# Optimization experiments

Measured on AMD Instinct MI355X. Metric: run time of the kernel, lower is better.

Reference implementation:

```python
import jax, jax.numpy as jnp
import numpy as np

B, S, D, H = 4, 2048, 1024, 16
HD = D // H  # head size = 64


def setup_inputs() -> dict:
    key = jax.random.key(0)
    ks = jax.random.split(key, 8)
    scale = 1.0 / np.sqrt(D)
    return {
        "q": jax.random.normal(ks[0], (B, S, D), jnp.float32),
        "k": jax.random.normal(ks[1], (B, S, D), jnp.float32),
        "v": jax.random.normal(ks[2], (B, S, D), jnp.float32),
        "mask": jnp.ones((B, 1, S), dtype=bool),
        "Wq": jax.random.normal(ks[3], (D, D), jnp.float32) * scale,
        "bq": jnp.zeros((D,), jnp.float32),
        "Wk": jax.random.normal(ks[4], (D, D), jnp.float32) * scale,
        "bk": jnp.zeros((D,), jnp.float32),
        "Wv": jax.random.normal(ks[5], (D, D), jnp.float32) * scale,
        "bv": jnp.zeros((D,), jnp.float32),
        "Wo": jax.random.normal(ks[6], (D, D), jnp.float32) * scale,
        "bo": jnp.zeros((D,), jnp.float32),
    }


def _split_heads(x):
    # [B, S, D] -> [B, H, S, HD]
    return x.reshape(B, -1, H, HD).transpose(0, 2, 1, 3)


def reference(q, k, v, mask, Wq, bq, Wk, bk, Wv, bv, Wo, bo):
    qh = _split_heads(q @ Wq + bq) / jnp.sqrt(jnp.asarray(HD, q.dtype))
    kh = _split_heads(k @ Wk + bk)
    vh = _split_heads(v @ Wv + bv)
    # scores: [B, H, Sq, Sk]
    scores = jnp.einsum("bhqd,bhkd->bhqk", qh, kh)
    neg_inf = jnp.asarray(-jnp.inf, scores.dtype)
    scores = jnp.where(mask[:, None, :, :], scores, neg_inf)
    attn = jax.nn.softmax(scores, axis=-1)
    # dropout p=0.0 -> identity (eval semantics)
    ctx = jnp.einsum("bhqk,bhkd->bhqd", attn, vh)
    ctx = ctx.transpose(0, 2, 1, 3).reshape(B, -1, D)
    return ctx @ Wo + bo
```

## Files before the change

kernel.cpp:

```cpp
#include <hip/hip_runtime.h>
#include <hip/hip_bf16.h>


typedef __bf16 bf16_t;
typedef __bf16 bf16x8 __attribute__((ext_vector_type(8)));
typedef __bf16 bf16x4 __attribute__((ext_vector_type(4)));
typedef float  floatx4 __attribute__((ext_vector_type(4)));

constexpr int B_ = 4, S_ = 2048, D_ = 1024, H_ = 16, HD_ = 64;
constexpr int M_ = B_ * S_;

#if defined(__has_builtin)
#if __has_builtin(__builtin_amdgcn_exp2f)
#define EXP2_RAW __builtin_amdgcn_exp2f
#endif
#endif
#ifndef EXP2_RAW
#define EXP2_RAW __builtin_exp2f
#endif

__device__ __forceinline__ void gll16(const void* gsrc, void* ldst) {
  __builtin_amdgcn_global_load_lds(
      (__attribute__((address_space(1))) void*)gsrc,
      (__attribute__((address_space(3))) void*)ldst, 16, 0, 0);
}

struct WPtrs { const float* src[4]; bf16_t* dst[4]; };

__global__ __launch_bounds__(256)
void transpose_cast_w(WPtrs p) {
  __shared__ float tile[64][65];
  const int m  = blockIdx.y;
  const int kt = blockIdx.x >> 4;
  const int nt = blockIdx.x & 15;
  const float* W  = p.src[m];
  bf16_t*      Wt = p.dst[m];
  const int t = threadIdx.x;
#pragma unroll
  for (int i = 0; i < 16; ++i) {
    int idx = i*256 + t;
    int r = idx >> 6, c = idx & 63;
    tile[r][c] = W[(kt*64 + r)*D_ + nt*64 + c];
  }
  __syncthreads();
#pragma unroll
  for (int i = 0; i < 16; ++i) {
    int idx = i*256 + t;
    int r = idx >> 6, c = idx & 63;
    Wt[(long)(nt*64 + r)*D_ + kt*64 + c] = (bf16_t)tile[c][r];
  }
}

struct ProjArgs {
  const float*  A[3];
  const bf16_t* Bt[3];
  const float*  bias[3];
  float         scale[3];
  void*         out[3];
  int           epi[3];
};

__global__ __launch_bounds__(256)
void proj_gemm(ProjArgs pa) {
  __shared__ alignas(16) bf16_t AsT[128*72];
  __shared__ alignas(16) char   Bs[128*64*2];

  const int z    = blockIdx.z;
  const int tid  = threadIdx.x;
  const int lane = tid & 63;
  const int w    = tid >> 6;
  const int quad = lane >> 4;
  const int l16  = lane & 15;
  const int wr   = w >> 1, wc = w & 1;
  const long row0 = (long)blockIdx.x * 128;
  const int  col0 = blockIdx.y * 128;

  const float*  A  = pa.A[z];
  const bf16_t* Bt = pa.Bt[z];

  floatx4 acc[4][4];
#pragma unroll
  for (int i = 0; i < 4; ++i)
#pragma unroll
    for (int j = 0; j < 4; ++j) { floatx4 zz = {0.f,0.f,0.f,0.f}; acc[i][j] = zz; }

  for (int kt = 0; kt < D_/64; ++kt) {
    const int k0 = kt * 64;
#pragma unroll
    for (int i = 0; i < 8; ++i) {
      int g = i*256 + tid;
      int r = g >> 4, c4 = g & 15;
      float4 f = *(const float4*)(A + (row0 + r)*D_ + k0 + c4*4);
      bf16x4 pk;
      pk[0]=(bf16_t)f.x; pk[1]=(bf16_t)f.y; pk[2]=(bf16_t)f.z; pk[3]=(bf16_t)f.w;
      *(bf16x4*)(AsT + r*72 + c4*4) = pk;
    }
#pragma unroll
    for (int it = 0; it < 4; ++it) {
      int chunk = it*4 + w;
      int g = chunk*64 + lane;
      int r = g >> 3, cs = g & 7;
      int cg = cs ^ (r & 7);
      gll16(Bt + (long)(col0 + r)*D_ + k0 + cg*8, Bs + chunk*1024);
    }
    __syncthreads();

#pragma unroll
    for (int ks = 0; ks < 2; ++ks) {
      bf16x8 a[4], b[4];
#pragma unroll
      for (int i = 0; i < 4; ++i) {
        int r = wr*64 + i*16 + l16;
        a[i] = *(const bf16x8*)(AsT + r*72 + (ks*4 + quad)*8);
      }
#pragma unroll
      for (int j = 0; j < 4; ++j) {
        int r = wc*64 + j*16 + l16;
        int c = ks*4 + quad;
        b[j] = *(const bf16x8*)(Bs + ((r*8) + (c ^ (r & 7)))*16);
      }
#pragma unroll
      for (int i = 0; i < 4; ++i)
#pragma unroll
        for (int j = 0; j < 4; ++j)
          acc[i][j] = __builtin_amdgcn_mfma_f32_16x16x32_bf16(a[i], b[j], acc[i][j], 0, 0, 0);
    }
    __syncthreads();
  }

  const float* bias = pa.bias[z];
  const float scale = pa.scale[z];
  if (pa.epi[z] == 0) {
    bf16_t* C = (bf16_t*)pa.out[z];
#pragma unroll
    for (int j = 0; j < 4; ++j) {
      int c = col0 + wc*64 + j*16 + l16;
      float bv = bias[c];
#pragma unroll
      for (int i = 0; i < 4; ++i) {
        long r = row0 + wr*64 + i*16 + quad*4;
#pragma unroll
        for (int rg = 0; rg < 4; ++rg)
          C[(r+rg)*D_ + c] = (bf16_t)((acc[i][j][rg] + bv) * scale);
      }
    }
  } else {
    bf16_t* VT = (bf16_t*)pa.out[z];
#pragma unroll
    for (int j = 0; j < 4; ++j) {
      int c  = col0 + wc*64 + j*16 + l16;
      int h  = c >> 6, hd = c & 63;
      float bv = bias[c];
#pragma unroll
      for (int i = 0; i < 4; ++i) {
        long r = row0 + wr*64 + i*16 + quad*4;
        int b = (int)(r >> 11), s = (int)(r & 2047);
        bf16x4 pk;
#pragma unroll
        for (int rg = 0; rg < 4; ++rg) pk[rg] = (bf16_t)(acc[i][j][rg] + bv);
        *(bf16x4*)(VT + ((long)((b*H_ + h)*HD_ + hd))*S_ + s) = pk;
      }
    }
  }
}

__global__ __launch_bounds__(256)
void out_gemm(const bf16_t* __restrict__ Ap, const bf16_t* __restrict__ Bt,
              const float* __restrict__ bias, float* __restrict__ Cp)
{
  __shared__ alignas(16) char smem[128*64*2 + 128*64*2];
  char* As = smem;
  char* Bs = smem + 128*64*2;

  const int tid  = threadIdx.x;
  const int lane = tid & 63;
  const int w    = tid >> 6;
  const int quad = lane >> 4;
  const int l16  = lane & 15;
  const int wr   = w >> 1, wc = w & 1;
  const long row0 = (long)blockIdx.x * 128;
  const int  col0 = blockIdx.y * 128;

  floatx4 acc[4][4];
#pragma unroll
  for (int i = 0; i < 4; ++i)
#pragma unroll
    for (int j = 0; j < 4; ++j) { floatx4 zz = {0.f,0.f,0.f,0.f}; acc[i][j] = zz; }

  for (int kt = 0; kt < D_/64; ++kt) {
    const int k0 = kt * 64;
#pragma unroll
    for (int it = 0; it < 4; ++it) {
      int chunk = it*4 + w;
      int g = chunk*64 + lane;
      int r = g >> 3, cs = g & 7;
      int cg = cs ^ (r & 7);
      gll16(Ap + (long)(row0 + r)*D_ + k0 + cg*8, As + chunk*1024);
    }
#pragma unroll
    for (int it = 0; it < 4; ++it) {
      int chunk = it*4 + w;
      int g = chunk*64 + lane;
      int r = g >> 3, cs = g & 7;
      int cg = cs ^ (r & 7);
      gll16(Bt + (long)(col0 + r)*D_ + k0 + cg*8, Bs + chunk*1024);
    }
    __syncthreads();

#pragma unroll
    for (int ks = 0; ks < 2; ++ks) {
      bf16x8 a[4], b[4];
#pragma unroll
      for (int i = 0; i < 4; ++i) {
        int r = wr*64 + i*16 + l16;
        int c = ks*4 + quad;
        a[i] = *(const bf16x8*)(As + ((r*8) + (c ^ (r & 7)))*16);
      }
#pragma unroll
      for (int j = 0; j < 4; ++j) {
        int r = wc*64 + j*16 + l16;
        int c = ks*4 + quad;
        b[j] = *(const bf16x8*)(Bs + ((r*8) + (c ^ (r & 7)))*16);
      }
#pragma unroll
      for (int i = 0; i < 4; ++i)
#pragma unroll
        for (int j = 0; j < 4; ++j)
          acc[i][j] = __builtin_amdgcn_mfma_f32_16x16x32_bf16(a[i], b[j], acc[i][j], 0, 0, 0);
    }
    __syncthreads();
  }

#pragma unroll
  for (int j = 0; j < 4; ++j) {
    int c = col0 + wc*64 + j*16 + l16;
    float bv = bias[c];
#pragma unroll
    for (int i = 0; i < 4; ++i) {
      long r = row0 + wr*64 + i*16 + quad*4;
#pragma unroll
      for (int rg = 0; rg < 4; ++rg)
        Cp[(r+rg)*D_ + c] = acc[i][j][rg] + bv;
    }
  }
}

__global__ __launch_bounds__(256, 2)
void attn(const bf16_t* __restrict__ Qp, const bf16_t* __restrict__ Kp,
          const bf16_t* __restrict__ VTg, bf16_t* __restrict__ Ctx)
{
  __shared__ alignas(16) bf16_t Ks [2][128*64];
  __shared__ alignas(16) bf16_t VTs[2][64*128];
  __shared__ alignas(16) bf16_t Ps [4][32*64];

  const int tid  = threadIdx.x;
  const int lane = tid & 63;
  const int w    = tid >> 6;
  const int quad = lane >> 4;
  const int l16  = lane & 15;

  const int h  = blockIdx.x;
  const int qt = blockIdx.y;
  const int b  = blockIdx.z;
  const int bh = b*H_ + h;
  const long rowQ0 = (long)b * S_ + qt*128;
  const int  colH  = h * HD_;

  bf16x8 qf[2][2];
#pragma unroll
  for (int ks = 0; ks < 2; ++ks)
#pragma unroll
    for (int qs = 0; qs < 2; ++qs)
      qf[ks][qs] = *(const bf16x8*)(Qp + (rowQ0 + w*32 + qs*16 + l16)*D_ + colH + ks*32 + quad*8);

  floatx4 O[4][2];
#pragma unroll
  for (int vb = 0; vb < 4; ++vb)
#pragma unroll
    for (int qs = 0; qs < 2; ++qs) { floatx4 zz = {0.f,0.f,0.f,0.f}; O[vb][qs] = zz; }
  float lsum[2] = {0.f, 0.f};

  bf16_t* Pw = &Ps[w][0];

  {
    const long rowK0 = (long)b * S_;
#pragma unroll
    for (int i = 0; i < 4; ++i) {
      int chunk = w*4 + i;
      int G = chunk*64 + lane;
      int r = G >> 3, cs = G & 7, cg = cs ^ (r & 7);
      gll16(Kp + (rowK0 + r)*D_ + colH + cg*8, (char*)Ks[0] + chunk*1024);
    }
#pragma unroll
    for (int i = 0; i < 4; ++i) {
      int chunk = w*4 + i;
      int G = chunk*64 + lane;
      int r = G >> 4, cs = G & 15, cg = cs ^ (r & 15);
      gll16(VTg + ((long)(bh*HD_ + r))*S_ + cg*8, (char*)VTs[0] + chunk*1024);
    }
  }

  for (int kt = 0; kt < S_/128; ++kt) {
    __syncthreads();
    const int bs = kt & 1;

    if (kt + 1 < S_/128) {
      const int  kn    = kt + 1, bn = kn & 1;
      const int  kv0n  = kn*128;
      const long rowK0 = (long)b * S_ + kv0n;
#pragma unroll
      for (int i = 0; i < 4; ++i) {
        int chunk = w*4 + i;
        int G = chunk*64 + lane;
        int r = G >> 3, cs = G & 7, cg = cs ^ (r & 7);
        gll16(Kp + (rowK0 + r)*D_ + colH + cg*8, (char*)Ks[bn] + chunk*1024);
      }
#pragma unroll
      for (int i = 0; i < 4; ++i) {
        int chunk = w*4 + i;
        int G = chunk*64 + lane;
        int r = G >> 4, cs = G & 15, cg = cs ^ (r & 15);
        gll16(VTg + ((long)(bh*HD_ + r))*S_ + kv0n + cg*8, (char*)VTs[bn] + chunk*1024);
      }
    }

    floatx4 sc[8][2];
#pragma unroll
    for (int nb = 0; nb < 8; ++nb)
#pragma unroll
      for (int qs = 0; qs < 2; ++qs) { floatx4 zz = {0.f,0.f,0.f,0.f}; sc[nb][qs] = zz; }
#pragma unroll
    for (int ks = 0; ks < 2; ++ks) {
#pragma unroll
      for (int nb = 0; nb < 8; ++nb) {
        bf16x8 a = *(const bf16x8*)(Ks[bs] + (nb*16 + l16)*64 + (((ks*4 + quad) ^ (l16 & 7))*8));
#pragma unroll
        for (int qs = 0; qs < 2; ++qs)
          sc[nb][qs] = __builtin_amdgcn_mfma_f32_16x16x32_bf16(a, qf[ks][qs], sc[nb][qs], 0, 0, 0);
      }
    }

#pragma unroll
    for (int half = 0; half < 2; ++half) {
#pragma unroll
      for (int nbl = 0; nbl < 4; ++nbl) {
        int nb = half*4 + nbl;
#pragma unroll
        for (int qs = 0; qs < 2; ++qs) {
          bf16x4 pk;
#pragma unroll
          for (int rg = 0; rg < 4; ++rg) {
            float p = EXP2_RAW(sc[nb][qs][rg]);
            lsum[qs] += p;
            pk[rg] = (bf16_t)p;
          }
          *(bf16x4*)(Pw + (qs*16 + l16)*64 + ((2*nbl + (quad >> 1)) ^ (l16 & 7))*8 + (quad & 1)*4) = pk;
        }
      }
#pragma unroll
      for (int kbl = 0; kbl < 2; ++kbl) {
        bf16x8 pf[2];
#pragma unroll
        for (int qs = 0; qs < 2; ++qs)
          pf[qs] = *(const bf16x8*)(Pw + (qs*16 + l16)*64 + (((kbl*4 + quad) ^ (l16 & 7))*8));
#pragma unroll
        for (int vb = 0; vb < 4; ++vb) {
          bf16x8 vf = *(const bf16x8*)(VTs[bs] + (vb*16 + l16)*128 + (((half*8 + kbl*4 + quad) ^ l16)*8));
#pragma unroll
          for (int qs = 0; qs < 2; ++qs)
            O[vb][qs] = __builtin_amdgcn_mfma_f32_16x16x32_bf16(pf[qs], vf, O[vb][qs], 0, 0, 0);
        }
      }
    }
  }

#pragma unroll
  for (int qs = 0; qs < 2; ++qs) {
    lsum[qs] += __shfl_xor(lsum[qs], 16);
    lsum[qs] += __shfl_xor(lsum[qs], 32);
  }
#pragma unroll
  for (int qs = 0; qs < 2; ++qs)
#pragma unroll
    for (int rg = 0; rg < 4; ++rg) {
      float lv  = __shfl(lsum[qs], (lane & 48) | (quad*4 + rg));
      float inv = 1.0f / lv;
      long  r   = rowQ0 + w*32 + qs*16 + quad*4 + rg;
#pragma unroll
      for (int vb = 0; vb < 4; ++vb)
        Ctx[r*D_ + colH + vb*16 + l16] = (bf16_t)(O[vb][qs][rg] * inv);
    }
}

extern "C" void kernel_launch(void* const* d_in, const int* in_sizes, int n_in,
                              void* d_out, int out_size, void* d_ws, size_t ws_size,
                              hipStream_t stream)
{
  (void)in_sizes; (void)n_in; (void)out_size; (void)ws_size;
  const float* q  = (const float*)d_in[0];
  const float* k  = (const float*)d_in[1];
  const float* v  = (const float*)d_in[2];
  const float* Wq = (const float*)d_in[4];
  const float* bq = (const float*)d_in[5];
  const float* Wk = (const float*)d_in[6];
  const float* bk = (const float*)d_in[7];
  const float* Wv = (const float*)d_in[8];
  const float* bv = (const float*)d_in[9];
  const float* Wo = (const float*)d_in[10];
  const float* bo = (const float*)d_in[11];

  char* ws = (char*)d_ws;
  bf16_t* WTq = (bf16_t*)(ws + ((size_t)0 << 20));
  bf16_t* WTk = (bf16_t*)(ws + ((size_t)2 << 20));
  bf16_t* WTv = (bf16_t*)(ws + ((size_t)4 << 20));
  bf16_t* WTo = (bf16_t*)(ws + ((size_t)6 << 20));
  bf16_t* QP  = (bf16_t*)(ws + ((size_t)8  << 20));
  bf16_t* KP  = (bf16_t*)(ws + ((size_t)24 << 20));
  bf16_t* VTg = (bf16_t*)(ws + ((size_t)40 << 20));
  bf16_t* CTX = (bf16_t*)(ws + ((size_t)56 << 20));

  WPtrs wp;
  wp.src[0] = Wq; wp.src[1] = Wk; wp.src[2] = Wv; wp.src[3] = Wo;
  wp.dst[0] = WTq; wp.dst[1] = WTk; wp.dst[2] = WTv; wp.dst[3] = WTo;
  transpose_cast_w<<<dim3(256, 4), 256, 0, stream>>>(wp);

  ProjArgs pa;
  pa.A[0] = q;  pa.A[1] = k;  pa.A[2] = v;
  pa.Bt[0] = WTq; pa.Bt[1] = WTk; pa.Bt[2] = WTv;
  pa.bias[0] = bq; pa.bias[1] = bk; pa.bias[2] = bv;
  pa.scale[0] = 1.4426950408889634f / 8.0f;
  pa.scale[1] = 1.0f; pa.scale[2] = 1.0f;
  pa.out[0] = QP; pa.out[1] = KP; pa.out[2] = VTg;
  pa.epi[0] = 0; pa.epi[1] = 0; pa.epi[2] = 1;
  proj_gemm<<<dim3(M_/128, D_/128, 3), 256, 0, stream>>>(pa);

  attn<<<dim3(H_, S_/128, B_), 256, 0, stream>>>(QP, KP, VTg, CTX);

  out_gemm<<<dim3(M_/128, D_/128), 256, 0, stream>>>(CTX, WTo, bo, (float*)d_out);
}
```

Before: 349.1 us.

## Precast QKV inputs to bf16 and use async LDS loads in projection GEMM

Adds a separate cast kernel that converts q, k, v to bf16 in workspace once, so the projection GEMM can load A tiles with direct global-to-LDS loads using a swizzled layout instead of reading fp32 and converting per tile. This removes the redundant fp32 reads and conversions repeated across the column blocks, at the cost of an extra pass over the inputs and more workspace. The output GEMM also shrinks its column tile from 128 to 64, doubling block count for occupancy. The new path runs only when the workspace is large enough, otherwise it falls back to the old path.

```diff
diff --git a/kernel.cpp b/kernel.cpp
--- a/kernel.cpp
+++ b/kernel.cpp
@@ -51,8 +51,27 @@
   }
 }
 
-struct ProjArgs {
-  const float*  A[3];
+struct CastArgs { const float* src[3]; bf16_t* dst[3]; };
+
+__global__ __launch_bounds__(256)
+void cast_qkv(CastArgs ca) {
+  const int gid = blockIdx.x*256 + threadIdx.x;
+#pragma unroll
+  for (int i = 0; i < 4; ++i) {
+    int g = gid + i*786432;
+    int t = g >> 20, o = g & 1048575;
+    const float* s = ca.src[t] + (long)o*8;
+    float4 f0 = *(const float4*)s;
+    float4 f1 = *(const float4*)(s + 4);
+    bf16x8 vv;
+    vv[0]=(bf16_t)f0.x; vv[1]=(bf16_t)f0.y; vv[2]=(bf16_t)f0.z; vv[3]=(bf16_t)f0.w;
+    vv[4]=(bf16_t)f1.x; vv[5]=(bf16_t)f1.y; vv[6]=(bf16_t)f1.z; vv[7]=(bf16_t)f1.w;
+    *(bf16x8*)(ca.dst[t] + (long)o*8) = vv;
+  }
+}
+
+struct ProjBF {
+  const bf16_t* A[3];
   const bf16_t* Bt[3];
   const float*  bias[3];
   float         scale[3];
@@ -61,9 +80,10 @@
 };
 
 __global__ __launch_bounds__(256)
-void proj_gemm(ProjArgs pa) {
-  __shared__ alignas(16) bf16_t AsT[128*72];
-  __shared__ alignas(16) char   Bs[128*64*2];
+void proj_gemm_bf16(ProjBF pa) {
+  __shared__ alignas(16) char smem[128*64*2 + 128*64*2];
+  char* As = smem;
+  char* Bs = smem + 128*64*2;
 
   const int z    = blockIdx.z;
   const int tid  = threadIdx.x;
@@ -75,7 +95,7 @@
   const long row0 = (long)blockIdx.x * 128;
   const int  col0 = blockIdx.y * 128;
 
-  const float*  A  = pa.A[z];
+  const bf16_t* A  = pa.A[z];
   const bf16_t* Bt = pa.Bt[z];
 
   floatx4 acc[4][4];
@@ -86,21 +106,18 @@
 
   for (int kt = 0; kt < D_/64; ++kt) {
     const int k0 = kt * 64;
-#pragma unroll
-    for (int i = 0; i < 8; ++i) {
-      int g = i*256 + tid;
-      int r = g >> 4, c4 = g & 15;
-      float4 f = *(const float4*)(A + (row0 + r)*D_ + k0 + c4*4);
-      bf16x4 pk;
-      pk[0]=(bf16_t)f.x; pk[1]=(bf16_t)f.y; pk[2]=(bf16_t)f.z; pk[3]=(bf16_t)f.w;
-      *(bf16x4*)(AsT + r*72 + c4*4) = pk;
-    }
 #pragma unroll
     for (int it = 0; it < 4; ++it) {
       int chunk = it*4 + w;
       int g = chunk*64 + lane;
-      int r = g >> 3, cs = g & 7;
-      int cg = cs ^ (r & 7);
+      int r = g >> 3, cs = g & 7, cg = cs ^ (r & 7);
+      gll16(A + (long)(row0 + r)*D_ + k0 + cg*8, As + chunk*1024);
+    }
+#pragma unroll
+    for (int it = 0; it < 4; ++it) {
+      int chunk = it*4 + w;
+      int g = chunk*64 + lane;
+      int r = g >> 3, cs = g & 7, cg = cs ^ (r & 7);
       gll16(Bt + (long)(col0 + r)*D_ + k0 + cg*8, Bs + chunk*1024);
     }
     __syncthreads();
@@ -111,7 +128,8 @@
 #pragma unroll
       for (int i = 0; i < 4; ++i) {
         int r = wr*64 + i*16 + l16;
-        a[i] = *(const bf16x8*)(AsT + r*72 + (ks*4 + quad)*8);
+        int c = ks*4 + quad;
+        a[i] = *(const bf16x8*)(As + ((r*8) + (c ^ (r & 7)))*16);
       }
 #pragma unroll
       for (int j = 0; j < 4; ++j) {
@@ -164,14 +182,21 @@
   }
 }
 
+struct ProjArgs {
+  const float*  A[3];
+  const bf16_t* Bt[3];
+  const float*  bias[3];
+  float         scale[3];
+  void*         out[3];
+  int           epi[3];
+};
+
 __global__ __launch_bounds__(256)
-void out_gemm(const bf16_t* __restrict__ Ap, const bf16_t* __restrict__ Bt,
-              const float* __restrict__ bias, float* __restrict__ Cp)
-{
-  __shared__ alignas(16) char smem[128*64*2 + 128*64*2];
-  char* As = smem;
-  char* Bs = smem + 128*64*2;
-
+void proj_gemm(ProjArgs pa) {
+  __shared__ alignas(16) bf16_t AsT[128*72];
+  __shared__ alignas(16) char   Bs[128*64*2];
+
+  const int z    = blockIdx.z;
   const int tid  = threadIdx.x;
   const int lane = tid & 63;
   const int w    = tid >> 6;
@@ -181,6 +206,9 @@
   const long row0 = (long)blockIdx.x * 128;
   const int  col0 = blockIdx.y * 128;
 
+  const float*  A  = pa.A[z];
+  const bf16_t* Bt = pa.Bt[z];
+
   floatx4 acc[4][4];
 #pragma unroll
   for (int i = 0; i < 4; ++i)
@@ -189,20 +217,20 @@
 
   for (int kt = 0; kt < D_/64; ++kt) {
     const int k0 = kt * 64;
+#pragma unroll
+    for (int i = 0; i < 8; ++i) {
+      int g = i*256 + tid;
+      int r = g >> 4, c4 = g & 15;
+      float4 f = *(const float4*)(A + (row0 + r)*D_ + k0 + c4*4);
+      bf16x4 pk;
+      pk[0]=(bf16_t)f.x; pk[1]=(bf16_t)f.y; pk[2]=(bf16_t)f.z; pk[3]=(bf16_t)f.w;
+      *(bf16x4*)(AsT + r*72 + c4*4) = pk;
+    }
 #pragma unroll
     for (int it = 0; it < 4; ++it) {
       int chunk = it*4 + w;
       int g = chunk*64 + lane;
-      int r = g >> 3, cs = g & 7;
-      int cg = cs ^ (r & 7);
-      gll16(Ap + (long)(row0 + r)*D_ + k0 + cg*8, As + chunk*1024);
-    }
-#pragma unroll
-    for (int it = 0; it < 4; ++it) {
-      int chunk = it*4 + w;
-      int g = chunk*64 + lane;
-      int r = g >> 3, cs = g & 7;
-      int cg = cs ^ (r & 7);
+      int r = g >> 3, cs = g & 7, cg = cs ^ (r & 7);
       gll16(Bt + (long)(col0 + r)*D_ + k0 + cg*8, Bs + chunk*1024);
     }
     __syncthreads();
@@ -213,8 +241,7 @@
 #pragma unroll
       for (int i = 0; i < 4; ++i) {
         int r = wr*64 + i*16 + l16;
-        int c = ks*4 + quad;
-        a[i] = *(const bf16x8*)(As + ((r*8) + (c ^ (r & 7)))*16);
+        a[i] = *(const bf16x8*)(AsT + r*72 + (ks*4 + quad)*8);
       }
 #pragma unroll
       for (int j = 0; j < 4; ++j) {
@@ -231,9 +258,110 @@
     __syncthreads();
   }
 
-#pragma unroll
-  for (int j = 0; j < 4; ++j) {
-    int c = col0 + wc*64 + j*16 + l16;
+  const float* bias = pa.bias[z];
+  const float scale = pa.scale[z];
+  if (pa.epi[z] == 0) {
+    bf16_t* C = (bf16_t*)pa.out[z];
+#pragma unroll
+    for (int j = 0; j < 4; ++j) {
+      int c = col0 + wc*64 + j*16 + l16;
+      float bv = bias[c];
+#pragma unroll
+      for (int i = 0; i < 4; ++i) {
+        long r = row0 + wr*64 + i*16 + quad*4;
+#pragma unroll
+        for (int rg = 0; rg < 4; ++rg)
+          C[(r+rg)*D_ + c] = (bf16_t)((acc[i][j][rg] + bv) * scale);
+      }
+    }
+  } else {
+    bf16_t* VT = (bf16_t*)pa.out[z];
+#pragma unroll
+    for (int j = 0; j < 4; ++j) {
+      int c  = col0 + wc*64 + j*16 + l16;
+      int h  = c >> 6, hd = c & 63;
+      float bv = bias[c];
+#pragma unroll
+      for (int i = 0; i < 4; ++i) {
+        long r = row0 + wr*64 + i*16 + quad*4;
+        int b = (int)(r >> 11), s = (int)(r & 2047);
+        bf16x4 pk;
+#pragma unroll
+        for (int rg = 0; rg < 4; ++rg) pk[rg] = (bf16_t)(acc[i][j][rg] + bv);
+        *(bf16x4*)(VT + ((long)((b*H_ + h)*HD_ + hd))*S_ + s) = pk;
+      }
+    }
+  }
+}
+
+__global__ __launch_bounds__(256)
+void out_gemm(const bf16_t* __restrict__ Ap, const bf16_t* __restrict__ Bt,
+              const float* __restrict__ bias, float* __restrict__ Cp)
+{
+  __shared__ alignas(16) char smem[128*64*2 + 64*64*2];
+  char* As = smem;
+  char* Bs = smem + 128*64*2;
+
+  const int tid  = threadIdx.x;
+  const int lane = tid & 63;
+  const int w    = tid >> 6;
+  const int quad = lane >> 4;
+  const int l16  = lane & 15;
+  const int wr   = w >> 1, wc = w & 1;
+  const long row0 = (long)blockIdx.x * 128;
+  const int  col0 = blockIdx.y * 64;
+
+  floatx4 acc[4][2];
+#pragma unroll
+  for (int i = 0; i < 4; ++i)
+#pragma unroll
+    for (int j = 0; j < 2; ++j) { floatx4 zz = {0.f,0.f,0.f,0.f}; acc[i][j] = zz; }
+
+  for (int kt = 0; kt < D_/64; ++kt) {
+    const int k0 = kt * 64;
+#pragma unroll
+    for (int it = 0; it < 4; ++it) {
+      int chunk = it*4 + w;
+      int g = chunk*64 + lane;
+      int r = g >> 3, cs = g & 7, cg = cs ^ (r & 7);
+      gll16(Ap + (long)(row0 + r)*D_ + k0 + cg*8, As + chunk*1024);
+    }
+#pragma unroll
+    for (int it = 0; it < 2; ++it) {
+      int chunk = it*4 + w;
+      int g = chunk*64 + lane;
+      int r = g >> 3, cs = g & 7, cg = cs ^ (r & 7);
+      gll16(Bt + (long)(col0 + r)*D_ + k0 + cg*8, Bs + chunk*1024);
+    }
+    __syncthreads();
+
+#pragma unroll
+    for (int ks = 0; ks < 2; ++ks) {
+      bf16x8 a[4], b[2];
+#pragma unroll
+      for (int i = 0; i < 4; ++i) {
+        int r = wr*64 + i*16 + l16;
+        int c = ks*4 + quad;
+        a[i] = *(const bf16x8*)(As + ((r*8) + (c ^ (r & 7)))*16);
+      }
+#pragma unroll
+      for (int j = 0; j < 2; ++j) {
+        int r = wc*32 + j*16 + l16;
+        int c = ks*4 + quad;
+        b[j] = *(const bf16x8*)(Bs + ((r*8) + (c ^ (r & 7)))*16);
+      }
+#pragma unroll
+      for (int i = 0; i < 4; ++i)
+#pragma unroll
+        for (int j = 0; j < 2; ++j)
+          acc[i][j] = __builtin_amdgcn_mfma_f32_16x16x32_bf16(a[i], b[j], acc[i][j], 0, 0, 0);
+    }
+    __syncthreads();
+  }
+
+#pragma unroll
+  for (int j = 0; j < 2; ++j) {
+    int c = col0 + wc*32 + j*16 + l16;
     float bv = bias[c];
 #pragma unroll
     for (int i = 0; i < 4; ++i) {
@@ -396,7 +524,7 @@
                               void* d_out, int out_size, void* d_ws, size_t ws_size,
                               hipStream_t stream)
 {
-  (void)in_sizes; (void)n_in; (void)out_size; (void)ws_size;
+  (void)in_sizes; (void)n_in; (void)out_size;
   const float* q  = (const float*)d_in[0];
   const float* k  = (const float*)d_in[1];
   const float* v  = (const float*)d_in[2];
@@ -414,27 +542,56 @@
   bf16_t* WTk = (bf16_t*)(ws + ((size_t)2 << 20));
   bf16_t* WTv = (bf16_t*)(ws + ((size_t)4 << 20));
   bf16_t* WTo = (bf16_t*)(ws + ((size_t)6 << 20));
-  bf16_t* QP  = (bf16_t*)(ws + ((size_t)8  << 20));
-  bf16_t* KP  = (bf16_t*)(ws + ((size_t)24 << 20));
-  bf16_t* VTg = (bf16_t*)(ws + ((size_t)40 << 20));
-  bf16_t* CTX = (bf16_t*)(ws + ((size_t)56 << 20));
 
   WPtrs wp;
   wp.src[0] = Wq; wp.src[1] = Wk; wp.src[2] = Wv; wp.src[3] = Wo;
   wp.dst[0] = WTq; wp.dst[1] = WTk; wp.dst[2] = WTv; wp.dst[3] = WTo;
   transpose_cast_w<<<dim3(256, 4), 256, 0, stream>>>(wp);
 
-  ProjArgs pa;
-  pa.A[0] = q;  pa.A[1] = k;  pa.A[2] = v;
-  pa.Bt[0] = WTq; pa.Bt[1] = WTk; pa.Bt[2] = WTv;
-  pa.bias[0] = bq; pa.bias[1] = bk; pa.bias[2] = bv;
-  pa.scale[0] = 1.4426950408889634f / 8.0f;
-  pa.scale[1] = 1.0f; pa.scale[2] = 1.0f;
-  pa.out[0] = QP; pa.out[1] = KP; pa.out[2] = VTg;
-  pa.epi[0] = 0; pa.epi[1] = 0; pa.epi[2] = 1;
-  proj_gemm<<<dim3(M_/128, D_/128, 3), 256, 0, stream>>>(pa);
-
-  attn<<<dim3(H_, S_/128, B_), 256, 0, stream>>>(QP, KP, VTg, CTX);
-
-  out_gemm<<<dim3(M_/128, D_/128), 256, 0, stream>>>(CTX, WTo, bo, (float*)d_out);
-}
+  const float qscale = 1.4426950408889634f / 8.0f;
+  const bool precast = (ws_size >= ((size_t)104 << 20));
+
+  if (precast) {
+    bf16_t* qb  = (bf16_t*)(ws + ((size_t)8  << 20));
+    bf16_t* kb  = (bf16_t*)(ws + ((size_t)24 << 20));
+    bf16_t* vb  = (bf16_t*)(ws + ((size_t)40 << 20));
+    bf16_t* QP  = (bf16_t*)(ws + ((size_t)56 << 20));
+    bf16_t* KP  = (bf16_t*)(ws + ((size_t)72 << 20));
+    bf16_t* VTg = (bf16_t*)(ws + ((size_t)88 << 20));
+    bf16_t* CTX = (bf16_t*)(ws + ((size_t)8  << 20));
+
+    CastArgs ca;
+    ca.src[0] = q; ca.src[1] = k; ca.src[2] = v;
+    ca.dst[0] = qb; ca.dst[1] = kb; ca.dst[2] = vb;
+    cast_qkv<<<3072, 256, 0, stream>>>(ca);
+
+    ProjBF pb;
+    pb.A[0] = qb; pb.A[1] = kb; pb.A[2] = vb;
+    pb.Bt[0] = WTq; pb.Bt[1] = WTk; pb.Bt[2] = WTv;
+    pb.bias[0] = bq; pb.bias[1] = bk; pb.bias[2] = bv;
+    pb.scale[0] = qscale; pb.scale[1] = 1.0f; pb.scale[2] = 1.0f;
+    pb.out[0] = QP; pb.out[1] = KP; pb.out[2] = VTg;
+    pb.epi[0] = 0; pb.epi[1] = 0; pb.epi[2] = 1;
+    proj_gemm_bf16<<<dim3(M_/128, D_/128, 3), 256, 0, stream>>>(pb);
+
+    attn<<<dim3(H_, S_/128, B_), 256, 0, stream>>>(QP, KP, VTg, CTX);
+    out_gemm<<<dim3(M_/128, D_/64), 256, 0, stream>>>(CTX, WTo, bo, (float*)d_out);
+  } else {
+    bf16_t* QP  = (bf16_t*)(ws + ((size_t)8  << 20));
+    bf16_t* KP  = (bf16_t*)(ws + ((size_t)24 << 20));
+    bf16_t* VTg = (bf16_t*)(ws + ((size_t)40 << 20));
+    bf16_t* CTX = (bf16_t*)(ws + ((size_t)56 << 20));
+
+    ProjArgs pa;
+    pa.A[0] = q;  pa.A[1] = k;  pa.A[2] = v;
+    pa.Bt[0] = WTq; pa.Bt[1] = WTk; pa.Bt[2] = WTv;
+    pa.bias[0] = bq; pa.bias[1] = bk; pa.bias[2] = bv;
+    pa.scale[0] = qscale; pa.scale[1] = 1.0f; pa.scale[2] = 1.0f;
+    pa.out[0] = QP; pa.out[1] = KP; pa.out[2] = VTg;
+    pa.epi[0] = 0; pa.epi[1] = 0; pa.epi[2] = 1;
+    proj_gemm<<<dim3(M_/128, D_/128, 3), 256, 0, stream>>>(pa);
+
+    attn<<<dim3(H_, S_/128, B_), 256, 0, stream>>>(QP, KP, VTg, CTX);
+    out_gemm<<<dim3(M_/128, D_/64), 256, 0, stream>>>(CTX, WTo, bo, (float*)d_out);
+  }
+}
```

Result: no change. 355.4 us (+1.8%).
